# Performance work log

Hardware: AMD Instinct MI355X
Metric: run time of the kernel (lower is better)

Reference implementation:

```python
import jax, jax.numpy as jnp
import numpy as np

B, T, C, HS = 8, 2048, 1024, 128


def setup_inputs() -> dict:
    key = jax.random.key(0)
    k1, k2, k3, k4 = jax.random.split(key, 4)
    return {
        "x": jax.random.normal(k1, (B, T, C), dtype=jnp.float32),
        "Wq": jax.random.normal(k2, (C, HS), dtype=jnp.float32) * (C ** -0.5),
        "Wk": jax.random.normal(k3, (C, HS), dtype=jnp.float32) * (C ** -0.5),
        "Wv": jax.random.normal(k4, (C, HS), dtype=jnp.float32) * (C ** -0.5),
    }


def _rope_tables(T, hs):
    # Matches get_rotary_embedding: d = hs//2, theta_i = 10000**(-2*(i-1)/d) for i in 0..d-1
    d = hs // 2
    i = jnp.arange(d, dtype=jnp.float32)
    theta = 10000.0 ** (-2.0 * (i - 1.0) / d)
    ang = jnp.arange(T, dtype=jnp.float32)[:, None] * theta[None, :]  # [T, d]
    return jnp.cos(ang), jnp.sin(ang)


def _rotate(t, c, s):
    # t: [B,T,hs]. Equivalent to t_m @ R_m with block-diag 2x2 rotations [[c,-s],[s,c]]:
    # out[2i] = e*c + o*s ; out[2i+1] = -e*s + o*c
    e, o = t[..., 0::2], t[..., 1::2]
    return jnp.stack([e * c + o * s, -e * s + o * c], axis=-1).reshape(t.shape)


def reference(x, Wq, Wk, Wv):
    Bx, Tx, Cx = x.shape
    hs = Wq.shape[1]
    c, s = _rope_tables(Tx, hs)
    q = _rotate(x @ Wq, c, s)  # [B,T,hs]
    k = _rotate(x @ Wk, c, s)
    v = x @ Wv
    scores = jnp.einsum("bqh,bkh->bqk", q, k) * (hs ** -0.5)  # [B,T,T]
    mask = jnp.tril(jnp.ones((Tx, Tx), dtype=bool))
    scores = jnp.where(mask, scores, -jnp.inf)
    A = jax.nn.softmax(scores, axis=-1)
    return jnp.einsum("bqk,bkh->bqh", A, v)
```

## Files before the change

### kernel.cpp

```cpp
#include <hip/hip_runtime.h>

typedef __bf16 bf16x8 __attribute__((ext_vector_type(8)));
typedef float f32x4 __attribute__((ext_vector_type(4)));

typedef const unsigned int __attribute__((address_space(1)))* gptr_t;
typedef unsigned int __attribute__((address_space(3)))* lptr_t;

static __device__ __forceinline__ unsigned short f2bf(float f){
  __bf16 h = (__bf16)f;
  return __builtin_bit_cast(unsigned short, h);
}
static __device__ __forceinline__ float bf2f(unsigned short h){
  unsigned int u = ((unsigned int)h) << 16;
  return __builtin_bit_cast(float, u);
}

__global__ __launch_bounds__(256) void k_prepw(const float* __restrict__ Wq,
                                               const float* __restrict__ Wk,
                                               const float* __restrict__ Wv,
                                               unsigned short* __restrict__ Wtb){
  int idx = blockIdx.x * 256 + threadIdx.x;
  int m = idx >> 10;
  int k = idx & 1023;
  const float* W = (m < 128) ? Wq : ((m < 256) ? Wk : Wv);
  int n = m & 127;
  Wtb[idx] = f2bf(W[k * 128 + n]);
}

#define QKV_BUFS 12288
__global__ __launch_bounds__(512) void k_qkv(const float* __restrict__ x,
                                             const unsigned short* __restrict__ Wtb,
                                             unsigned short* __restrict__ Qr,
                                             unsigned short* __restrict__ Kr,
                                             unsigned short* __restrict__ Vt){
  __shared__ __align__(16) unsigned short lds[2 * QKV_BUFS];

  int bid0 = blockIdx.x;
  int wg = (bid0 & 7) * 96 + (bid0 >> 3);
  int mblk = wg / 3;
  int nblk = wg - mblk * 3;

  int tid = threadIdx.x;
  int lane = tid & 63, wid = tid >> 6;
  int wm = wid >> 1, wn = wid & 1;
  int g = lane >> 4, lr = lane & 15;

  f32x4 acc[4] = {};
  const float* xbase = x + (size_t)(mblk * 64) * 1024;
  const unsigned short* wbase = Wtb + (size_t)(nblk * 128) * 1024;

  int ar = tid >> 3, ac = tid & 7;
  const float* agp = xbase + (size_t)ar * 1024 + ac * 8;
  int awoff = ar * 128 + ((ac ^ (ar & 7)) << 4);
  int bp = tid & 7;
  int br1 = tid >> 3, br2 = br1 + 64;
  const unsigned short* bgp1 = wbase + (size_t)br1 * 1024 + ((bp ^ (br1 & 7)) << 3);
  const unsigned short* bgp2 = wbase + (size_t)br2 * 1024 + ((bp ^ (br2 & 7)) << 3);
  int bdoff1 = wid * 512;
  int bdoff2 = 4096 + wid * 512;

  {
    unsigned short* sB = lds + 4096;
    __builtin_amdgcn_global_load_lds((gptr_t)(const void*)bgp1,
                                     (lptr_t)(void*)(sB + bdoff1), 16, 0, 0);
    __builtin_amdgcn_global_load_lds((gptr_t)(const void*)bgp2,
                                     (lptr_t)(void*)(sB + bdoff2), 16, 0, 0);
    float4 v0 = *reinterpret_cast<const float4*>(agp);
    float4 v1 = *reinterpret_cast<const float4*>(agp + 4);
    union { bf16x8 h; uint4 u4; } pk;
    pk.h[0] = (__bf16)v0.x; pk.h[1] = (__bf16)v0.y;
    pk.h[2] = (__bf16)v0.z; pk.h[3] = (__bf16)v0.w;
    pk.h[4] = (__bf16)v1.x; pk.h[5] = (__bf16)v1.y;
    pk.h[6] = (__bf16)v1.z; pk.h[7] = (__bf16)v1.w;
    *reinterpret_cast<uint4*>((char*)lds + awoff) = pk.u4;
    __syncthreads();
  }

  int cur = 0;
  float4 fa0, fa1;
  for (int t = 0; t < 16; t++){
    if (t < 15){
      int k0n = (t + 1) * 64;
      unsigned short* sB = lds + (cur ^ 1) * QKV_BUFS + 4096;
      __builtin_amdgcn_global_load_lds((gptr_t)(const void*)(bgp1 + k0n),
                                       (lptr_t)(void*)(sB + bdoff1), 16, 0, 0);
      __builtin_amdgcn_global_load_lds((gptr_t)(const void*)(bgp2 + k0n),
                                       (lptr_t)(void*)(sB + bdoff2), 16, 0, 0);
      fa0 = *reinterpret_cast<const float4*>(agp + k0n);
      fa1 = *reinterpret_cast<const float4*>(agp + k0n + 4);
    }

    {
      const char* cA = (const char*)(lds + cur * QKV_BUFS);
      const char* cB = cA + 8192;
      int arow = wm * 16 + lr;
      int asw = (arow & 7) << 4;
#pragma unroll
      for (int ks = 0; ks < 2; ks++){
        bf16x8 af = *reinterpret_cast<const bf16x8*>(
            cA + arow * 128 + ((ks * 64 + g * 16) ^ asw));
#pragma unroll
        for (int n = 0; n < 4; n++){
          int brow = wn * 64 + n * 16 + lr;
          bf16x8 bn = *reinterpret_cast<const bf16x8*>(
              cB + brow * 128 + ((ks * 64 + g * 16) ^ ((brow & 7) << 4)));
          acc[n] = __builtin_amdgcn_mfma_f32_16x16x32_bf16(af, bn, acc[n], 0, 0, 0);
        }
      }
    }

    if (t < 15){
      union { bf16x8 h; uint4 u4; } pk;
      pk.h[0] = (__bf16)fa0.x; pk.h[1] = (__bf16)fa0.y;
      pk.h[2] = (__bf16)fa0.z; pk.h[3] = (__bf16)fa0.w;
      pk.h[4] = (__bf16)fa1.x; pk.h[5] = (__bf16)fa1.y;
      pk.h[6] = (__bf16)fa1.z; pk.h[7] = (__bf16)fa1.w;
      *reinterpret_cast<uint4*>((char*)(lds + (cur ^ 1) * QKV_BUFS) + awoff) = pk.u4;
    }
    __syncthreads();
    cur ^= 1;
  }

  int row0 = mblk * 64;
  if (nblk < 2){
    unsigned short* sE = lds;
    float scale = nblk ? 1.0f : 0.12751744950370064f;
#pragma unroll
    for (int n = 0; n < 4; n++){
      int col = wn * 64 + n * 16 + lr;
      int i = col >> 1;
      float theta = exp2f(13.287712379549449f * (2.0f - 2.0f * (float)i) * 0.015625f);
      float sgn = (lr & 1) ? -1.0f : 1.0f;
#pragma unroll
      for (int r = 0; r < 4; r++){
        int tl = wm * 16 + g * 4 + r;
        int t = (row0 + tl) & 2047;
        float s, c;
        sincosf((float)t * theta, &s, &c);
        float v = acc[n][r];
        float partner = __shfl_xor(v, 1);
        float res = (v * c + partner * sgn * s) * scale;
        sE[tl * 136 + col] = f2bf(res);
      }
    }
    __syncthreads();
    unsigned short* dst = (nblk ? Kr : Qr) + (size_t)row0 * 128;
#pragma unroll
    for (int p = 0; p < 2; p++){
      int u = tid + p * 512;
      int tl = u >> 4, h0 = (u & 15) * 8;
      uint4 vv = *reinterpret_cast<const uint4*>(&sE[tl * 136 + h0]);
      *reinterpret_cast<uint4*>(dst + (size_t)tl * 128 + h0) = vv;
    }
  } else {
    unsigned short* sE = lds;
#pragma unroll
    for (int n = 0; n < 4; n++){
      int col = wn * 64 + n * 16 + lr;
#pragma unroll
      for (int r = 0; r < 4; r++){
        int tl = wm * 16 + g * 4 + r;
        sE[col * 72 + tl] = f2bf(acc[n][r]);
      }
    }
    __syncthreads();
    int b = row0 >> 11;
    int t0 = row0 & 2047;
#pragma unroll
    for (int p = 0; p < 2; p++){
      int u = tid + p * 512;
      int h = u >> 3, tc = (u & 7) * 8;
      uint4 vv = *reinterpret_cast<const uint4*>(&sE[h * 72 + tc]);
      *reinterpret_cast<uint4*>(Vt + ((size_t)(b * 128 + h)) * 2048 + t0 + tc) = vv;
    }
  }
}

__global__ __launch_bounds__(128) void k_attn_part(const unsigned short* __restrict__ Qr,
                                                   const unsigned short* __restrict__ Kr,
                                                   const unsigned short* __restrict__ Vt,
                                                   unsigned short* __restrict__ Opart,
                                                   float* __restrict__ ml){
  __shared__ __align__(16) unsigned short sK[32][136];
  __shared__ __align__(16) unsigned short sV[128][40];
  __shared__ __align__(16) unsigned short sP[2][16][40];

  int bid = blockIdx.x;
  int b = bid / 160;
  int rem = bid - b * 160;
  int qt, c;
  if (rem < 16)      { qt = rem;                    c = 0; }
  else if (rem < 48) { qt = 16 + ((rem - 16) >> 1); c = (rem - 16) & 1; }
  else if (rem < 96) { int r2 = rem - 48; int d = r2 / 3; qt = 32 + d; c = r2 - 3 * d; }
  else               { int r3 = rem - 96; qt = 48 + (r3 >> 2); c = r3 & 3; }

  int q_base = qt * 32;
  int kv_start = c * 512;
  int kv_end = min(kv_start + 512, q_base + 32);
  int niter = (kv_end - kv_start) >> 5;

  int tid = threadIdx.x, w = tid >> 6, lane = tid & 63;
  int g = lane >> 4, lr = lane & 15;

  int qrow = q_base + w * 16 + lr;
  const unsigned short* qptr = Qr + ((size_t)(b * 2048 + qrow)) * 128;
  bf16x8 qf[4];
#pragma unroll
  for (int hc = 0; hc < 4; hc++)
    qf[hc] = *reinterpret_cast<const bf16x8*>(qptr + hc * 32 + g * 8);

  f32x4 oacc[8] = {};
  float mrow = -1e30f, lrow = 0.0f;

  const unsigned short* Kb = Kr + (size_t)b * 2048 * 128;
  const unsigned short* Vb = Vt + (size_t)b * 128 * 2048;

  for (int it = 0; it < niter; it++){
    int kv0 = kv_start + it * 32;
    __syncthreads();
#pragma unroll
    for (int p = 0; p < 4; p++){
      int idx = tid + p * 128;
      int r = idx >> 4, c8 = (idx & 15) * 8;
      *reinterpret_cast<uint4*>(&sK[r][c8]) =
        *reinterpret_cast<const uint4*>(Kb + (size_t)(kv0 + r) * 128 + c8);
    }
#pragma unroll
    for (int p = 0; p < 4; p++){
      int idx = tid + p * 128;
      int h = idx >> 2, c8 = (idx & 3) * 8;
      *reinterpret_cast<uint4*>(&sV[h][c8]) =
        *reinterpret_cast<const uint4*>(Vb + (size_t)h * 2048 + kv0 + c8);
    }
    __syncthreads();

    f32x4 st[2];
#pragma unroll
    for (int ct = 0; ct < 2; ct++){
      f32x4 a = {0.f, 0.f, 0.f, 0.f};
#pragma unroll
      for (int hc = 0; hc < 4; hc++){
        bf16x8 kf = *reinterpret_cast<const bf16x8*>(&sK[ct * 16 + lr][hc * 32 + g * 8]);
        a = __builtin_amdgcn_mfma_f32_16x16x32_bf16(kf, qf[hc], a, 0, 0, 0);
      }
      st[ct] = a;
    }

    float mx = -1e30f;
#pragma unroll
    for (int ct = 0; ct < 2; ct++){
      int kvb = kv0 + ct * 16 + g * 4;
#pragma unroll
      for (int r = 0; r < 4; r++){
        float s = (kvb + r <= qrow) ? st[ct][r] : -1e30f;
        st[ct][r] = s;
        mx = fmaxf(mx, s);
      }
    }
    mx = fmaxf(mx, __shfl_xor(mx, 16));
    mx = fmaxf(mx, __shfl_xor(mx, 32));
    float m = fmaxf(mrow, mx);
    float alpha = exp2f(mrow - m);

    float rs = 0.0f;
#pragma unroll
    for (int ct = 0; ct < 2; ct++){
      float p0 = exp2f(st[ct][0] - m);
      float p1 = exp2f(st[ct][1] - m);
      float p2 = exp2f(st[ct][2] - m);
      float p3 = exp2f(st[ct][3] - m);
      rs += (p0 + p1) + (p2 + p3);
      uint2 pk;
      pk.x = ((unsigned int)f2bf(p1) << 16) | f2bf(p0);
      pk.y = ((unsigned int)f2bf(p3) << 16) | f2bf(p2);
      *reinterpret_cast<uint2*>(&sP[w][lr][ct * 16 + g * 4]) = pk;
    }
    rs += __shfl_xor(rs, 16);
    rs += __shfl_xor(rs, 32);
    lrow = lrow * alpha + rs;
    mrow = m;

    float af0 = __shfl(alpha, g * 4 + 0);
    float af1 = __shfl(alpha, g * 4 + 1);
    float af2 = __shfl(alpha, g * 4 + 2);
    float af3 = __shfl(alpha, g * 4 + 3);
#pragma unroll
    for (int ht = 0; ht < 8; ht++){
      oacc[ht][0] *= af0;
      oacc[ht][1] *= af1;
      oacc[ht][2] *= af2;
      oacc[ht][3] *= af3;
    }

    bf16x8 pa = *reinterpret_cast<const bf16x8*>(&sP[w][lr][g * 8]);
#pragma unroll
    for (int ht = 0; ht < 8; ht++){
      bf16x8 vf = *reinterpret_cast<const bf16x8*>(&sV[ht * 16 + lr][g * 8]);
      oacc[ht] = __builtin_amdgcn_mfma_f32_16x16x32_bf16(pa, vf, oacc[ht], 0, 0, 0);
    }
  }

  size_t slot = (size_t)(b * 64 + qt) * 4 + c;
  unsigned short* op = Opart + slot * 4096;
  float* mlp = ml + slot * 64;
#pragma unroll
  for (int ht = 0; ht < 8; ht++)
#pragma unroll
    for (int r = 0; r < 4; r++){
      int rowl = w * 16 + g * 4 + r;
      op[rowl * 128 + ht * 16 + lr] = f2bf(oacc[ht][r]);
    }
  if (lane < 16){
    mlp[w * 16 + lr]      = mrow;
    mlp[32 + w * 16 + lr] = lrow;
  }
}

__global__ __launch_bounds__(256) void k_comb(const unsigned short* __restrict__ Opart,
                                              const float* __restrict__ ml,
                                              float* __restrict__ out){
  int bid = blockIdx.x;
  int b = bid >> 6, qt = bid & 63;
  int nck = (qt >> 4) + 1;
  int tid = threadIdx.x;
  int row = tid >> 3;
  int col0 = (tid & 7) * 16;
  size_t slot0 = (size_t)(b * 64 + qt) * 4;

  float m_c[4], l_c[4];
  float M = -1e30f;
#pragma unroll
  for (int c = 0; c < 4; c++) if (c < nck){
    m_c[c] = ml[(slot0 + c) * 64 + row];
    l_c[c] = ml[(slot0 + c) * 64 + 32 + row];
    M = fmaxf(M, m_c[c]);
  }
  float L = 0.0f, wgt[4];
#pragma unroll
  for (int c = 0; c < 4; c++) if (c < nck){
    wgt[c] = exp2f(m_c[c] - M);
    L += wgt[c] * l_c[c];
  }
  float acc[16] = {};
#pragma unroll
  for (int c = 0; c < 4; c++) if (c < nck){
    const unsigned short* src = Opart + (slot0 + c) * 4096 + row * 128 + col0;
    uint4 u0 = *reinterpret_cast<const uint4*>(src);
    uint4 u1 = *reinterpret_cast<const uint4*>(src + 8);
    unsigned int uu[8] = {u0.x, u0.y, u0.z, u0.w, u1.x, u1.y, u1.z, u1.w};
#pragma unroll
    for (int j = 0; j < 8; j++){
      acc[2 * j]     += wgt[c] * bf2f((unsigned short)(uu[j] & 0xFFFF));
      acc[2 * j + 1] += wgt[c] * bf2f((unsigned short)(uu[j] >> 16));
    }
  }
  float invL = 1.0f / L;
  float* dst = out + ((size_t)(b * 2048 + qt * 32 + row)) * 128 + col0;
#pragma unroll
  for (int j = 0; j < 4; j++){
    float4 v = {acc[4 * j] * invL, acc[4 * j + 1] * invL,
                acc[4 * j + 2] * invL, acc[4 * j + 3] * invL};
    *reinterpret_cast<float4*>(dst + 4 * j) = v;
  }
}

extern "C" void kernel_launch(void* const* d_in, const int* in_sizes, int n_in,
                              void* d_out, int out_size, void* d_ws, size_t ws_size,
                              hipStream_t stream) {
  const float* x  = (const float*)d_in[0];
  const float* Wq = (const float*)d_in[1];
  const float* Wk = (const float*)d_in[2];
  const float* Wv = (const float*)d_in[3];
  float* out = (float*)d_out;

  char* ws = (char*)d_ws;
  unsigned short* Wtb   = (unsigned short*)ws;
  unsigned short* Qr    = (unsigned short*)(ws + 786432);
  unsigned short* Kr    = (unsigned short*)(ws + 786432 + 4194304);
  unsigned short* Vt    = (unsigned short*)(ws + 786432 + 2*4194304);
  unsigned short* Opart = (unsigned short*)(ws + 786432 + 3*4194304);
  float* ml             = (float*)(ws + 786432 + 3*4194304 + 16777216);

  hipLaunchKernelGGL(k_prepw, dim3(1536), dim3(256), 0, stream, Wq, Wk, Wv, Wtb);
  hipLaunchKernelGGL(k_qkv,   dim3(768),  dim3(512), 0, stream, x, Wtb, Qr, Kr, Vt);
  hipLaunchKernelGGL(k_attn_part, dim3(1280), dim3(128), 0, stream, Qr, Kr, Vt, Opart, ml);
  hipLaunchKernelGGL(k_comb, dim3(512), dim3(256), 0, stream, Opart, ml, out);
}
```

Baseline: 76.28 us.

## Enlarge QKV projection tile to 128x128 per workgroup with 4x4 MFMA accumulators

The QKV GEMM kernel now computes a 128-row by 128-column tile per workgroup with 4 waves. Each wave holds a 4x4 grid of MFMA accumulators, instead of 8 waves each holding a 1x4 grid over 64 rows. Each loaded B fragment is reused across four A fragments. The A tile uses a padded stride in place of an XOR swizzle. The grid drops from 768 to 384 workgroups, with larger LDS buffers and more register pressure. This raises arithmetic intensity per LDS and global load, but lowers occupancy and parallelism across the 256 CUs.

```diff
diff --git a/kernel.cpp b/kernel.cpp
--- a/kernel.cpp
+++ b/kernel.cpp
@@ -27,8 +27,8 @@
   Wtb[idx] = f2bf(W[k * 128 + n]);
 }
 
-#define QKV_BUFS 12288
-__global__ __launch_bounds__(512) void k_qkv(const float* __restrict__ x,
+#define QKV_BUFS 17408
+__global__ __launch_bounds__(256) void k_qkv(const float* __restrict__ x,
                                              const unsigned short* __restrict__ Wtb,
                                              unsigned short* __restrict__ Qr,
                                              unsigned short* __restrict__ Kr,
@@ -36,7 +36,7 @@
   __shared__ __align__(16) unsigned short lds[2 * QKV_BUFS];
 
   int bid0 = blockIdx.x;
-  int wg = (bid0 & 7) * 96 + (bid0 >> 3);
+  int wg = (bid0 & 7) * 48 + (bid0 >> 3);
   int mblk = wg / 3;
   int nblk = wg - mblk * 3;
 
@@ -45,83 +45,100 @@
   int wm = wid >> 1, wn = wid & 1;
   int g = lane >> 4, lr = lane & 15;
 
-  f32x4 acc[4] = {};
-  const float* xbase = x + (size_t)(mblk * 64) * 1024;
+  f32x4 acc[4][4] = {};
+  const float* xbase = x + (size_t)(mblk * 128) * 1024;
   const unsigned short* wbase = Wtb + (size_t)(nblk * 128) * 1024;
 
-  int ar = tid >> 3, ac = tid & 7;
-  const float* agp = xbase + (size_t)ar * 1024 + ac * 8;
-  int awoff = ar * 128 + ((ac ^ (ar & 7)) << 4);
-  int bp = tid & 7;
-  int br1 = tid >> 3, br2 = br1 + 64;
-  const unsigned short* bgp1 = wbase + (size_t)br1 * 1024 + ((bp ^ (br1 & 7)) << 3);
-  const unsigned short* bgp2 = wbase + (size_t)br2 * 1024 + ((bp ^ (br2 & 7)) << 3);
-  int bdoff1 = wid * 512;
-  int bdoff2 = 4096 + wid * 512;
+  int ar = tid >> 1, ah = (tid & 1) * 32;
+  const float* agp = xbase + (size_t)ar * 1024 + ah;
+  int awbyte = ar * 144 + (tid & 1) * 64;
+  int bp = lane & 7;
+  int br0 = wid * 32 + (lane >> 3);
+  int bswz = (bp ^ (br0 & 7)) << 3;
+  int bdofs = 9216 + wid * 2048;
 
   {
-    unsigned short* sB = lds + 4096;
-    __builtin_amdgcn_global_load_lds((gptr_t)(const void*)bgp1,
-                                     (lptr_t)(void*)(sB + bdoff1), 16, 0, 0);
-    __builtin_amdgcn_global_load_lds((gptr_t)(const void*)bgp2,
-                                     (lptr_t)(void*)(sB + bdoff2), 16, 0, 0);
-    float4 v0 = *reinterpret_cast<const float4*>(agp);
-    float4 v1 = *reinterpret_cast<const float4*>(agp + 4);
-    union { bf16x8 h; uint4 u4; } pk;
-    pk.h[0] = (__bf16)v0.x; pk.h[1] = (__bf16)v0.y;
-    pk.h[2] = (__bf16)v0.z; pk.h[3] = (__bf16)v0.w;
-    pk.h[4] = (__bf16)v1.x; pk.h[5] = (__bf16)v1.y;
-    pk.h[6] = (__bf16)v1.z; pk.h[7] = (__bf16)v1.w;
-    *reinterpret_cast<uint4*>((char*)lds + awoff) = pk.u4;
+#pragma unroll
+    for (int i = 0; i < 4; i++)
+      __builtin_amdgcn_global_load_lds(
+        (gptr_t)(const void*)(wbase + (size_t)(br0 + i * 8) * 1024 + bswz),
+        (lptr_t)(void*)(lds + bdofs + i * 512), 16, 0, 0);
+    float4 fa[8];
+#pragma unroll
+    for (int j = 0; j < 8; j++)
+      fa[j] = *reinterpret_cast<const float4*>(agp + 4 * j);
+#pragma unroll
+    for (int c = 0; c < 4; c++){
+      union { bf16x8 h; uint4 u4; } pk;
+      float4 v0 = fa[2 * c], v1 = fa[2 * c + 1];
+      pk.h[0] = (__bf16)v0.x; pk.h[1] = (__bf16)v0.y;
+      pk.h[2] = (__bf16)v0.z; pk.h[3] = (__bf16)v0.w;
+      pk.h[4] = (__bf16)v1.x; pk.h[5] = (__bf16)v1.y;
+      pk.h[6] = (__bf16)v1.z; pk.h[7] = (__bf16)v1.w;
+      *reinterpret_cast<uint4*>((char*)lds + awbyte + c * 16) = pk.u4;
+    }
     __syncthreads();
   }
 
   int cur = 0;
-  float4 fa0, fa1;
   for (int t = 0; t < 16; t++){
+    float4 fa[8];
     if (t < 15){
       int k0n = (t + 1) * 64;
-      unsigned short* sB = lds + (cur ^ 1) * QKV_BUFS + 4096;
-      __builtin_amdgcn_global_load_lds((gptr_t)(const void*)(bgp1 + k0n),
-                                       (lptr_t)(void*)(sB + bdoff1), 16, 0, 0);
-      __builtin_amdgcn_global_load_lds((gptr_t)(const void*)(bgp2 + k0n),
-                                       (lptr_t)(void*)(sB + bdoff2), 16, 0, 0);
-      fa0 = *reinterpret_cast<const float4*>(agp + k0n);
-      fa1 = *reinterpret_cast<const float4*>(agp + k0n + 4);
+      unsigned short* nb = lds + (cur ^ 1) * QKV_BUFS;
+#pragma unroll
+      for (int i = 0; i < 4; i++)
+        __builtin_amdgcn_global_load_lds(
+          (gptr_t)(const void*)(wbase + (size_t)(br0 + i * 8) * 1024 + k0n + bswz),
+          (lptr_t)(void*)(nb + bdofs + i * 512), 16, 0, 0);
+#pragma unroll
+      for (int j = 0; j < 8; j++)
+        fa[j] = *reinterpret_cast<const float4*>(agp + k0n + 4 * j);
     }
 
     {
       const char* cA = (const char*)(lds + cur * QKV_BUFS);
-      const char* cB = cA + 8192;
-      int arow = wm * 16 + lr;
-      int asw = (arow & 7) << 4;
+      const char* cB = cA + 18432;
 #pragma unroll
       for (int ks = 0; ks < 2; ks++){
-        bf16x8 af = *reinterpret_cast<const bf16x8*>(
-            cA + arow * 128 + ((ks * 64 + g * 16) ^ asw));
+        bf16x8 af[4], bf[4];
+#pragma unroll
+        for (int m = 0; m < 4; m++){
+          int arow = wm * 64 + m * 16 + lr;
+          af[m] = *reinterpret_cast<const bf16x8*>(cA + arow * 144 + ks * 64 + g * 16);
+        }
 #pragma unroll
         for (int n = 0; n < 4; n++){
           int brow = wn * 64 + n * 16 + lr;
-          bf16x8 bn = *reinterpret_cast<const bf16x8*>(
+          bf[n] = *reinterpret_cast<const bf16x8*>(
               cB + brow * 128 + ((ks * 64 + g * 16) ^ ((brow & 7) << 4)));
-          acc[n] = __builtin_amdgcn_mfma_f32_16x16x32_bf16(af, bn, acc[n], 0, 0, 0);
         }
+#pragma unroll
+        for (int m = 0; m < 4; m++)
+#pragma unroll
+          for (int n = 0; n < 4; n++)
+            acc[m][n] = __builtin_amdgcn_mfma_f32_16x16x32_bf16(af[m], bf[n], acc[m][n], 0, 0, 0);
       }
     }
 
     if (t < 15){
-      union { bf16x8 h; uint4 u4; } pk;
-      pk.h[0] = (__bf16)fa0.x; pk.h[1] = (__bf16)fa0.y;
-      pk.h[2] = (__bf16)fa0.z; pk.h[3] = (__bf16)fa0.w;
-      pk.h[4] = (__bf16)fa1.x; pk.h[5] = (__bf16)fa1.y;
-      pk.h[6] = (__bf16)fa1.z; pk.h[7] = (__bf16)fa1.w;
-      *reinterpret_cast<uint4*>((char*)(lds + (cur ^ 1) * QKV_BUFS) + awoff) = pk.u4;
+      char* dA = (char*)(lds + (cur ^ 1) * QKV_BUFS);
+#pragma unroll
+      for (int c = 0; c < 4; c++){
+        union { bf16x8 h; uint4 u4; } pk;
+        float4 v0 = fa[2 * c], v1 = fa[2 * c + 1];
+        pk.h[0] = (__bf16)v0.x; pk.h[1] = (__bf16)v0.y;
+        pk.h[2] = (__bf16)v0.z; pk.h[3] = (__bf16)v0.w;
+        pk.h[4] = (__bf16)v1.x; pk.h[5] = (__bf16)v1.y;
+        pk.h[6] = (__bf16)v1.z; pk.h[7] = (__bf16)v1.w;
+        *reinterpret_cast<uint4*>(dA + awbyte + c * 16) = pk.u4;
+      }
     }
     __syncthreads();
     cur ^= 1;
   }
 
-  int row0 = mblk * 64;
+  int row0 = mblk * 128;
   if (nblk < 2){
     unsigned short* sE = lds;
     float scale = nblk ? 1.0f : 0.12751744950370064f;
@@ -132,22 +149,24 @@
       float theta = exp2f(13.287712379549449f * (2.0f - 2.0f * (float)i) * 0.015625f);
       float sgn = (lr & 1) ? -1.0f : 1.0f;
 #pragma unroll
-      for (int r = 0; r < 4; r++){
-        int tl = wm * 16 + g * 4 + r;
-        int t = (row0 + tl) & 2047;
-        float s, c;
-        sincosf((float)t * theta, &s, &c);
-        float v = acc[n][r];
-        float partner = __shfl_xor(v, 1);
-        float res = (v * c + partner * sgn * s) * scale;
-        sE[tl * 136 + col] = f2bf(res);
-      }
+      for (int m = 0; m < 4; m++)
+#pragma unroll
+        for (int r = 0; r < 4; r++){
+          int tl = wm * 64 + m * 16 + g * 4 + r;
+          int t = (row0 + tl) & 2047;
+          float s, c;
+          sincosf((float)t * theta, &s, &c);
+          float v = acc[m][n][r];
+          float partner = __shfl_xor(v, 1);
+          float res = (v * c + partner * sgn * s) * scale;
+          sE[tl * 136 + col] = f2bf(res);
+        }
     }
     __syncthreads();
     unsigned short* dst = (nblk ? Kr : Qr) + (size_t)row0 * 128;
 #pragma unroll
-    for (int p = 0; p < 2; p++){
-      int u = tid + p * 512;
+    for (int p = 0; p < 8; p++){
+      int u = tid + p * 256;
       int tl = u >> 4, h0 = (u & 15) * 8;
       uint4 vv = *reinterpret_cast<const uint4*>(&sE[tl * 136 + h0]);
       *reinterpret_cast<uint4*>(dst + (size_t)tl * 128 + h0) = vv;
@@ -158,19 +177,21 @@
     for (int n = 0; n < 4; n++){
       int col = wn * 64 + n * 16 + lr;
 #pragma unroll
-      for (int r = 0; r < 4; r++){
-        int tl = wm * 16 + g * 4 + r;
-        sE[col * 72 + tl] = f2bf(acc[n][r]);
-      }
+      for (int m = 0; m < 4; m++)
+#pragma unroll
+        for (int r = 0; r < 4; r++){
+          int tl = wm * 64 + m * 16 + g * 4 + r;
+          sE[col * 136 + tl] = f2bf(acc[m][n][r]);
+        }
     }
     __syncthreads();
     int b = row0 >> 11;
     int t0 = row0 & 2047;
 #pragma unroll
-    for (int p = 0; p < 2; p++){
-      int u = tid + p * 512;
-      int h = u >> 3, tc = (u & 7) * 8;
-      uint4 vv = *reinterpret_cast<const uint4*>(&sE[h * 72 + tc]);
+    for (int p = 0; p < 8; p++){
+      int u = tid + p * 256;
+      int h = u >> 4, tc = (u & 15) * 8;
+      uint4 vv = *reinterpret_cast<const uint4*>(&sE[h * 136 + tc]);
       *reinterpret_cast<uint4*>(Vt + ((size_t)(b * 128 + h)) * 2048 + t0 + tc) = vv;
     }
   }
@@ -382,7 +403,7 @@
   float* ml             = (float*)(ws + 786432 + 3*4194304 + 16777216);
 
   hipLaunchKernelGGL(k_prepw, dim3(1536), dim3(256), 0, stream, Wq, Wk, Wv, Wtb);
-  hipLaunchKernelGGL(k_qkv,   dim3(768),  dim3(512), 0, stream, x, Wtb, Qr, Kr, Vt);
+  hipLaunchKernelGGL(k_qkv,   dim3(384),  dim3(256), 0, stream, x, Wtb, Qr, Kr, Vt);
   hipLaunchKernelGGL(k_attn_part, dim3(1280), dim3(128), 0, stream, Qr, Kr, Vt, Opart, ml);
   hipLaunchKernelGGL(k_comb, dim3(512), dim3(256), 0, stream, Opart, ml, out);
 }
```

Result: slower. 265.5 us (+248.1%).
